# Performance work log

Measured on AMD Instinct MI355X. Metric: run time of the kernel, lower is better.

The kernel has to match this reference:

```python
import jax, jax.numpy as jnp
import numpy as np

LN_EPS = 1e-5


def setup_inputs() -> dict:
    key = jax.random.key(0)
    ks = jax.random.split(key, 4)
    B, S, H, R = 8, 4096, 1024, 64
    hidden_states = jax.random.normal(ks[0], (B, S, H), dtype=jnp.float32)
    w_down = jax.random.normal(ks[1], (H, R), dtype=jnp.float32) * (1.0 / np.sqrt(H))
    b_down = jnp.zeros((R,), dtype=jnp.float32)
    w_up = jax.random.normal(ks[2], (R, H), dtype=jnp.float32) * (1.0 / np.sqrt(R))
    b_up = jnp.zeros((H,), dtype=jnp.float32)
    ln_gamma = jnp.ones((H,), dtype=jnp.float32)
    ln_beta = jnp.zeros((H,), dtype=jnp.float32)
    return {
        "hidden_states": hidden_states,
        "ln_gamma": ln_gamma,
        "ln_beta": ln_beta,
        "w_down": w_down,
        "b_down": b_down,
        "w_up": w_up,
        "b_up": b_up,
    }


def _layernorm(x, gamma, beta):
    mu = jnp.mean(x, axis=-1, keepdims=True)
    var = jnp.mean(jnp.square(x - mu), axis=-1, keepdims=True)
    return (x - mu) * jax.lax.rsqrt(var + LN_EPS) * gamma + beta


def reference(hidden_states, ln_gamma, ln_beta, w_down, b_down, w_up, b_up):
    # pre-norm adapter: LN -> down-proj -> gelu -> up-proj -> +residual
    res = hidden_states
    h = _layernorm(hidden_states, ln_gamma, ln_beta)
    h = jnp.einsum("bsh,hr->bsr", h, w_down) + b_down
    h = jax.nn.gelu(h, approximate=False)  # torch GELU (exact erf form)
    h = jnp.einsum("bsr,rh->bsh", h, w_up) + b_up
    return h + res
```

## Files before the change

kernel.cpp:

```cpp
#include <hip/hip_runtime.h>
#include <hip/hip_bf16.h>
#include <math.h>

#define H 1024
#define R 64
#define BM 16
#define NTHREADS 256
#define TSTRIDE 72

typedef __attribute__((ext_vector_type(8))) short short8;
typedef __attribute__((ext_vector_type(4))) float floatx4;

__device__ __forceinline__ unsigned short f2bf(float f) {
    unsigned int u = __builtin_bit_cast(unsigned int, f);
    u += 0x7fffu + ((u >> 16) & 1u);
    return (unsigned short)(u >> 16);
}

__global__ void prep_weights(const float* __restrict__ w_down,
                             const float* __restrict__ w_up,
                             unsigned short* __restrict__ wsd,
                             unsigned short* __restrict__ wsu) {
    int tid = blockIdx.x * blockDim.x + threadIdx.x;
    int j    = tid & 7;
    int lane = (tid >> 3) & 63;
    int f    = tid >> 9;
    int b = lane >> 4, p = lane & 15;
    {
        int kk = f >> 2, n = f & 3;
        int row = kk * 32 + b * 8 + j;
        int col = n * 16 + p;
        wsd[tid] = f2bf(w_down[row * R + col]);
    }
    {
        int ks = f >> 6, n = f & 63;
        int row = ks * 32 + b * 8 + j;
        int col = n * 16 + p;
        wsu[tid] = f2bf(w_up[row * H + col]);
    }
}

__global__ __launch_bounds__(NTHREADS, 4)
void adapter_kernel(const float* __restrict__ x,
                    const float* __restrict__ gamma,
                    const float* __restrict__ beta,
                    const float* __restrict__ b_down,
                    const float* __restrict__ b_up,
                    const unsigned short* __restrict__ wsd,
                    const unsigned short* __restrict__ wsu,
                    float* __restrict__ out) {
    __shared__ __align__(16) unsigned short y_lds[BM * H];
    __shared__ __align__(16) unsigned short t_lds[BM * TSTRIDE];

    const int tid  = threadIdx.x;
    const int lane = tid & 63;
    const int wave = tid >> 6;
    const long rowbase = (long)blockIdx.x * BM;

    float gg[16], bb[16];
    {
        const floatx4* g4 = (const floatx4*)(gamma + lane * 16);
        const floatx4* b4 = (const floatx4*)(beta  + lane * 16);
        #pragma unroll
        for (int q = 0; q < 4; ++q) {
            floatx4 gv = g4[q], bv = b4[q];
            #pragma unroll
            for (int e = 0; e < 4; ++e) { gg[q*4+e] = gv[e]; bb[q*4+e] = bv[e]; }
        }
    }
    #pragma unroll 2
    for (int i = 0; i < 4; ++i) {
        int r = wave * 4 + i;
        const floatx4* xr = (const floatx4*)(x + (rowbase + r) * H + lane * 16);
        float v[16];
        #pragma unroll
        for (int q = 0; q < 4; ++q) {
            floatx4 xv = xr[q];
            #pragma unroll
            for (int e = 0; e < 4; ++e) v[q*4+e] = xv[e];
        }
        float s1 = 0.f, s2 = 0.f;
        #pragma unroll
        for (int q = 0; q < 16; ++q) { s1 += v[q]; s2 += v[q] * v[q]; }
        #pragma unroll
        for (int off = 32; off >= 1; off >>= 1) {
            s1 += __shfl_xor(s1, off);
            s2 += __shfl_xor(s2, off);
        }
        float mu  = s1 * (1.0f / (float)H);
        float var = s2 * (1.0f / (float)H) - mu * mu;
        float rs  = rsqrtf(var + 1e-5f);
        int c = r & 7;
        short8 lo, hi;
        #pragma unroll
        for (int q = 0; q < 8; ++q) lo[q] = (short)f2bf((v[q]     - mu) * rs * gg[q]     + bb[q]);
        #pragma unroll
        for (int q = 0; q < 8; ++q) hi[q] = (short)f2bf((v[q + 8] - mu) * rs * gg[q + 8] + bb[q + 8]);
        int s0  = (2 * lane)     ^ c;
        int s1g = (2 * lane + 1) ^ c;
        *(short8*)&y_lds[r * H + s0  * 8] = lo;
        *(short8*)&y_lds[r * H + s1g * 8] = hi;
    }
    __syncthreads();

    const int p = lane & 15;
    const int b = lane >> 4;

    floatx4 acc = {0.f, 0.f, 0.f, 0.f};
    const int asw = p & 7;
    const short8* wsd8 = (const short8*)wsd;
    #pragma unroll 4
    for (int kk = 0; kk < 32; ++kk) {
        int gidx = 4 * kk + b;
        short8 a  = *(const short8*)&y_lds[p * H + ((gidx ^ asw) * 8)];
        short8 b0 = wsd8[(kk * 4 + wave) * 64 + lane];
        acc = __builtin_amdgcn_mfma_f32_16x16x32_bf16(a, b0, acc, 0, 0, 0);
    }
    {
        float bd = b_down[16 * wave + p];
        #pragma unroll
        for (int reg = 0; reg < 4; ++reg) {
            int trow = b * 4 + reg;
            float u = acc[reg] + bd;
            u = 0.5f * u * (1.0f + erff(u * 0.70710678f));
            t_lds[trow * TSTRIDE + 16 * wave + p] = f2bf(u);
        }
    }
    __syncthreads();

    short8 a0 = *(const short8*)&t_lds[p * TSTRIDE + b * 8];
    short8 a1 = *(const short8*)&t_lds[p * TSTRIDE + 32 + b * 8];
    const short8* wsu8 = (const short8*)wsu;

    #pragma unroll 2
    for (int nn = 0; nn < 16; ++nn) {
        int n = 16 * wave + nn;
        short8 bu0 = wsu8[(n)      * 64 + lane];
        short8 bu1 = wsu8[(64 + n) * 64 + lane];
        floatx4 av = {0.f, 0.f, 0.f, 0.f};
        av = __builtin_amdgcn_mfma_f32_16x16x32_bf16(a0, bu0, av, 0, 0, 0);
        av = __builtin_amdgcn_mfma_f32_16x16x32_bf16(a1, bu1, av, 0, 0, 0);
        int col = n * 16 + p;
        float bup = b_up[col];
        #pragma unroll
        for (int reg = 0; reg < 4; ++reg) {
            long rr = rowbase + b * 4 + reg;
            out[rr * H + col] = av[reg] + bup + x[rr * H + col];
        }
    }
}

extern "C" void kernel_launch(void* const* d_in, const int* in_sizes, int n_in,
                              void* d_out, int out_size, void* d_ws, size_t ws_size,
                              hipStream_t stream) {
    const float* x      = (const float*)d_in[0];
    const float* gamma  = (const float*)d_in[1];
    const float* beta   = (const float*)d_in[2];
    const float* w_down = (const float*)d_in[3];
    const float* b_down = (const float*)d_in[4];
    const float* w_up   = (const float*)d_in[5];
    const float* b_up   = (const float*)d_in[6];
    float* out = (float*)d_out;

    unsigned short* wsd = (unsigned short*)d_ws;
    unsigned short* wsu = wsd + 65536;

    int M = in_sizes[0] / H;
    prep_weights<<<256, 256, 0, stream>>>(w_down, w_up, wsd, wsu);
    adapter_kernel<<<M / BM, NTHREADS, 0, stream>>>(x, gamma, beta, b_down, b_up,
                                                    wsd, wsu, out);
}
```

Measured before the change: 268.7 us.

## Fold LayerNorm into down-projection weights and split K across waves

Rewrites the down-projection so the raw input x (in bf16) multiplies gamma-scaled weights directly, and applies LayerNorm algebraically afterward as rs*(acc - mu*sum(gamma*w)) + (beta*w + b_down). The normalized row no longer has to be written to and read back from LDS. Each wave now handles a quarter of the hidden dimension for all 64 rows, with partial sums reduced through LDS. The block tile grows from 16 to 64 rows and occupancy drops to 2 blocks per SM. Rounding raw x to bf16 before subtracting the mean, together with the single-pass variance, may cost accuracy when inputs have a large mean.

After: 279.4 us. 1.04x slower.

```diff
diff --git a/kernel.cpp b/kernel.cpp
--- a/kernel.cpp
+++ b/kernel.cpp
@@ -4,9 +4,10 @@
 
 #define H 1024
 #define R 64
-#define BM 16
+#define BM 64
 #define NTHREADS 256
 #define TSTRIDE 72
+#define PSTRIDE 20
 
 typedef __attribute__((ext_vector_type(8))) short short8;
 typedef __attribute__((ext_vector_type(4))) float floatx4;
@@ -19,6 +20,7 @@
 
 __global__ void prep_weights(const float* __restrict__ w_down,
                              const float* __restrict__ w_up,
+                             const float* __restrict__ gamma,
                              unsigned short* __restrict__ wsd,
                              unsigned short* __restrict__ wsu) {
     int tid = blockIdx.x * blockDim.x + threadIdx.x;
@@ -30,7 +32,7 @@
         int kk = f >> 2, n = f & 3;
         int row = kk * 32 + b * 8 + j;
         int col = n * 16 + p;
-        wsd[tid] = f2bf(w_down[row * R + col]);
+        wsd[tid] = f2bf(gamma[row] * w_down[row * R + col]);
     }
     {
         int ks = f >> 6, n = f & 63;
@@ -40,112 +42,176 @@
     }
 }
 
-__global__ __launch_bounds__(NTHREADS, 4)
+__global__ void prep_vec(const float* __restrict__ w_down,
+                         const float* __restrict__ gamma,
+                         const float* __restrict__ beta,
+                         const float* __restrict__ b_down,
+                         float* __restrict__ w1, float* __restrict__ c0) {
+    int r = blockIdx.x;
+    int t = threadIdx.x;
+    float a = 0.f, c = 0.f;
+    for (int h = t; h < H; h += NTHREADS) {
+        float wd = w_down[h * R + r];
+        a += gamma[h] * wd;
+        c += beta[h] * wd;
+    }
+    #pragma unroll
+    for (int off = 32; off >= 1; off >>= 1) {
+        a += __shfl_xor(a, off);
+        c += __shfl_xor(c, off);
+    }
+    __shared__ float red[8];
+    int wv = t >> 6;
+    if ((t & 63) == 0) { red[wv] = a; red[4 + wv] = c; }
+    __syncthreads();
+    if (t == 0) {
+        w1[r] = red[0] + red[1] + red[2] + red[3];
+        c0[r] = red[4] + red[5] + red[6] + red[7] + b_down[r];
+    }
+}
+
+__global__ __launch_bounds__(NTHREADS, 2)
 void adapter_kernel(const float* __restrict__ x,
-                    const float* __restrict__ gamma,
-                    const float* __restrict__ beta,
-                    const float* __restrict__ b_down,
                     const float* __restrict__ b_up,
                     const unsigned short* __restrict__ wsd,
                     const unsigned short* __restrict__ wsu,
+                    const float* __restrict__ w1v,
+                    const float* __restrict__ c0v,
                     float* __restrict__ out) {
-    __shared__ __align__(16) unsigned short y_lds[BM * H];
+    __shared__ __align__(16) float part[12 * 64 * PSTRIDE];
     __shared__ __align__(16) unsigned short t_lds[BM * TSTRIDE];
+    __shared__ float s1w[4][BM], s2w[4][BM];
 
     const int tid  = threadIdx.x;
     const int lane = tid & 63;
-    const int wave = tid >> 6;
+    const int w    = tid >> 6;
+    const int p    = lane & 15;
+    const int b    = lane >> 4;
     const long rowbase = (long)blockIdx.x * BM;
-
-    float gg[16], bb[16];
-    {
-        const floatx4* g4 = (const floatx4*)(gamma + lane * 16);
-        const floatx4* b4 = (const floatx4*)(beta  + lane * 16);
-        #pragma unroll
-        for (int q = 0; q < 4; ++q) {
-            floatx4 gv = g4[q], bv = b4[q];
-            #pragma unroll
-            for (int e = 0; e < 4; ++e) { gg[q*4+e] = gv[e]; bb[q*4+e] = bv[e]; }
-        }
-    }
-    #pragma unroll 2
-    for (int i = 0; i < 4; ++i) {
-        int r = wave * 4 + i;
-        const floatx4* xr = (const floatx4*)(x + (rowbase + r) * H + lane * 16);
-        float v[16];
-        #pragma unroll
-        for (int q = 0; q < 4; ++q) {
-            floatx4 xv = xr[q];
-            #pragma unroll
-            for (int e = 0; e < 4; ++e) v[q*4+e] = xv[e];
-        }
-        float s1 = 0.f, s2 = 0.f;
-        #pragma unroll
-        for (int q = 0; q < 16; ++q) { s1 += v[q]; s2 += v[q] * v[q]; }
-        #pragma unroll
-        for (int off = 32; off >= 1; off >>= 1) {
-            s1 += __shfl_xor(s1, off);
-            s2 += __shfl_xor(s2, off);
-        }
-        float mu  = s1 * (1.0f / (float)H);
-        float var = s2 * (1.0f / (float)H) - mu * mu;
-        float rs  = rsqrtf(var + 1e-5f);
-        int c = r & 7;
-        short8 lo, hi;
-        #pragma unroll
-        for (int q = 0; q < 8; ++q) lo[q] = (short)f2bf((v[q]     - mu) * rs * gg[q]     + bb[q]);
-        #pragma unroll
-        for (int q = 0; q < 8; ++q) hi[q] = (short)f2bf((v[q + 8] - mu) * rs * gg[q + 8] + bb[q + 8]);
-        int s0  = (2 * lane)     ^ c;
-        int s1g = (2 * lane + 1) ^ c;
-        *(short8*)&y_lds[r * H + s0  * 8] = lo;
-        *(short8*)&y_lds[r * H + s1g * 8] = hi;
+    const int kbase = w * 256;
+
+    float s1[4] = {0.f,0.f,0.f,0.f}, s2[4] = {0.f,0.f,0.f,0.f};
+    floatx4 acc[4][4];
+    #pragma unroll
+    for (int mt = 0; mt < 4; ++mt)
+        #pragma unroll
+        for (int nt = 0; nt < 4; ++nt)
+            acc[mt][nt] = floatx4{0.f,0.f,0.f,0.f};
+
+    const short8* wsd8 = (const short8*)wsd;
+    #pragma unroll
+    for (int kt = 0; kt < 8; ++kt) {
+        short8 af[4];
+        #pragma unroll
+        for (int mt = 0; mt < 4; ++mt) {
+            const float* px = x + (rowbase + mt * 16 + p) * H + kbase + kt * 32 + b * 8;
+            floatx4 v0 = *(const floatx4*)px;
+            floatx4 v1 = *(const floatx4*)(px + 4);
+            short8 a;
+            #pragma unroll
+            for (int e = 0; e < 4; ++e) {
+                s1[mt] += v0[e] + v1[e];
+                s2[mt] += v0[e] * v0[e] + v1[e] * v1[e];
+                a[e]     = (short)f2bf(v0[e]);
+                a[4 + e] = (short)f2bf(v1[e]);
+            }
+            af[mt] = a;
+        }
+        #pragma unroll
+        for (int nt = 0; nt < 4; ++nt) {
+            short8 bfrag = wsd8[(size_t)((w * 8 + kt) * 4 + nt) * 64 + lane];
+            #pragma unroll
+            for (int mt = 0; mt < 4; ++mt)
+                acc[mt][nt] = __builtin_amdgcn_mfma_f32_16x16x32_bf16(af[mt], bfrag, acc[mt][nt], 0, 0, 0);
+        }
+    }
+
+    #pragma unroll
+    for (int mt = 0; mt < 4; ++mt) {
+        s1[mt] += __shfl_xor(s1[mt], 16); s1[mt] += __shfl_xor(s1[mt], 32);
+        s2[mt] += __shfl_xor(s2[mt], 16); s2[mt] += __shfl_xor(s2[mt], 32);
+    }
+    if (b == 0) {
+        #pragma unroll
+        for (int mt = 0; mt < 4; ++mt) {
+            s1w[w][mt * 16 + p] = s1[mt];
+            s2w[w][mt * 16 + p] = s2[mt];
+        }
+    }
+
+    floatx4 own[4];
+    #pragma unroll
+    for (int mt = 0; mt < 4; ++mt) {
+        if (mt != w) {
+            int idx = w * 3 + (mt < w ? mt : mt - 1);
+            float* dst = &part[idx * 64 * PSTRIDE];
+            #pragma unroll
+            for (int nt = 0; nt < 4; ++nt)
+                *(floatx4*)&dst[(nt * 16 + p) * PSTRIDE + b * 4] = acc[mt][nt];
+        } else {
+            #pragma unroll
+            for (int nt = 0; nt < 4; ++nt) own[nt] = acc[mt][nt];
+        }
     }
     __syncthreads();
 
-    const int p = lane & 15;
-    const int b = lane >> 4;
-
-    floatx4 acc = {0.f, 0.f, 0.f, 0.f};
-    const int asw = p & 7;
-    const short8* wsd8 = (const short8*)wsd;
-    #pragma unroll 4
-    for (int kk = 0; kk < 32; ++kk) {
-        int gidx = 4 * kk + b;
-        short8 a  = *(const short8*)&y_lds[p * H + ((gidx ^ asw) * 8)];
-        short8 b0 = wsd8[(kk * 4 + wave) * 64 + lane];
-        acc = __builtin_amdgcn_mfma_f32_16x16x32_bf16(a, b0, acc, 0, 0, 0);
-    }
-    {
-        float bd = b_down[16 * wave + p];
+    #pragma unroll
+    for (int src = 0; src < 3; ++src) {
+        int ow  = (src < w) ? src : src + 1;
+        int idx = ow * 3 + (w < ow ? w : w - 1);
+        const float* sp = &part[idx * 64 * PSTRIDE];
+        #pragma unroll
+        for (int nt = 0; nt < 4; ++nt)
+            own[nt] += *(const floatx4*)&sp[(nt * 16 + p) * PSTRIDE + b * 4];
+    }
+    float mu[4], rs[4];
+    #pragma unroll
+    for (int reg = 0; reg < 4; ++reg) {
+        int row = w * 16 + b * 4 + reg;
+        float a = s1w[0][row] + s1w[1][row] + s1w[2][row] + s1w[3][row];
+        float q = s2w[0][row] + s2w[1][row] + s2w[2][row] + s2w[3][row];
+        float m = a * (1.0f / (float)H);
+        float var = q * (1.0f / (float)H) - m * m;
+        mu[reg] = m;
+        rs[reg] = rsqrtf(var + 1e-5f);
+    }
+    #pragma unroll
+    for (int nt = 0; nt < 4; ++nt) {
+        float wv1 = w1v[nt * 16 + p];
+        float cv0 = c0v[nt * 16 + p];
         #pragma unroll
         for (int reg = 0; reg < 4; ++reg) {
-            int trow = b * 4 + reg;
-            float u = acc[reg] + bd;
+            float u = rs[reg] * (own[nt][reg] - mu[reg] * wv1) + cv0;
             u = 0.5f * u * (1.0f + erff(u * 0.70710678f));
-            t_lds[trow * TSTRIDE + 16 * wave + p] = f2bf(u);
+            t_lds[(w * 16 + b * 4 + reg) * TSTRIDE + nt * 16 + p] = f2bf(u);
         }
     }
     __syncthreads();
 
-    short8 a0 = *(const short8*)&t_lds[p * TSTRIDE + b * 8];
-    short8 a1 = *(const short8*)&t_lds[p * TSTRIDE + 32 + b * 8];
+    short8 a0[4], a1[4];
+    #pragma unroll
+    for (int mt = 0; mt < 4; ++mt) {
+        a0[mt] = *(const short8*)&t_lds[(mt * 16 + p) * TSTRIDE + b * 8];
+        a1[mt] = *(const short8*)&t_lds[(mt * 16 + p) * TSTRIDE + 32 + b * 8];
+    }
     const short8* wsu8 = (const short8*)wsu;
-
     #pragma unroll 2
     for (int nn = 0; nn < 16; ++nn) {
-        int n = 16 * wave + nn;
-        short8 bu0 = wsu8[(n)      * 64 + lane];
-        short8 bu1 = wsu8[(64 + n) * 64 + lane];
-        floatx4 av = {0.f, 0.f, 0.f, 0.f};
-        av = __builtin_amdgcn_mfma_f32_16x16x32_bf16(a0, bu0, av, 0, 0, 0);
-        av = __builtin_amdgcn_mfma_f32_16x16x32_bf16(a1, bu1, av, 0, 0, 0);
+        int n = w * 16 + nn;
+        short8 bu0 = wsu8[(size_t)n * 64 + lane];
+        short8 bu1 = wsu8[(size_t)(64 + n) * 64 + lane];
         int col = n * 16 + p;
         float bup = b_up[col];
         #pragma unroll
-        for (int reg = 0; reg < 4; ++reg) {
-            long rr = rowbase + b * 4 + reg;
-            out[rr * H + col] = av[reg] + bup + x[rr * H + col];
+        for (int mt = 0; mt < 4; ++mt) {
+            floatx4 av = {0.f, 0.f, 0.f, 0.f};
+            av = __builtin_amdgcn_mfma_f32_16x16x32_bf16(a0[mt], bu0, av, 0, 0, 0);
+            av = __builtin_amdgcn_mfma_f32_16x16x32_bf16(a1[mt], bu1, av, 0, 0, 0);
+            #pragma unroll
+            for (int reg = 0; reg < 4; ++reg) {
+                long rr = rowbase + mt * 16 + b * 4 + reg;
+                out[rr * H + col] = av[reg] + bup + x[rr * H + col];
+            }
         }
     }
 }
@@ -164,9 +230,11 @@
 
     unsigned short* wsd = (unsigned short*)d_ws;
     unsigned short* wsu = wsd + 65536;
+    float* w1 = (float*)(wsu + 65536);
+    float* c0 = w1 + 64;
 
     int M = in_sizes[0] / H;
-    prep_weights<<<256, 256, 0, stream>>>(w_down, w_up, wsd, wsu);
-    adapter_kernel<<<M / BM, NTHREADS, 0, stream>>>(x, gamma, beta, b_down, b_up,
-                                                    wsd, wsu, out);
-}
+    prep_weights<<<256, 256, 0, stream>>>(w_down, w_up, gamma, wsd, wsu);
+    prep_vec<<<64, 256, 0, stream>>>(w_down, gamma, beta, b_down, w1, c0);
+    adapter_kernel<<<M / BM, NTHREADS, 0, stream>>>(x, b_up, wsd, wsu, w1, c0, out);
+}
```

## Fold LayerNorm into down-projection weights and compute GEMM directly from raw input

Applied to the files above, without the earlier changes.

LayerNorm's gamma is folded into the down-projection weights, and beta with the bias into a per-column constant. The down GEMM now runs on raw bf16-converted x, and mean/rstd are applied afterwards as a rank-1 correction (rs*(acc - mu*w1) + c0). This removes the normalized-activation LDS staging buffer and a block barrier. Each wave now owns 16 rows with 64 rows per block, and a new small prep kernel computes the folded vectors. The risk is extra precision loss, because raw x goes to bf16 before the mean is subtracted, so the subtraction happens after the bf16 GEMM.

Result: slower. 289.2 us (+7.6%).

```diff
diff --git a/kernel.cpp b/kernel.cpp
--- a/kernel.cpp
+++ b/kernel.cpp
@@ -4,8 +4,9 @@
 
 #define H 1024
 #define R 64
-#define BM 16
 #define NTHREADS 256
+#define ROWS_PER_WAVE 16
+#define ROWS_PER_BLOCK 64
 #define TSTRIDE 72
 
 typedef __attribute__((ext_vector_type(8))) short short8;
@@ -19,6 +20,7 @@
 
 __global__ void prep_weights(const float* __restrict__ w_down,
                              const float* __restrict__ w_up,
+                             const float* __restrict__ gamma,
                              unsigned short* __restrict__ wsd,
                              unsigned short* __restrict__ wsu) {
     int tid = blockIdx.x * blockDim.x + threadIdx.x;
@@ -30,7 +32,7 @@
         int kk = f >> 2, n = f & 3;
         int row = kk * 32 + b * 8 + j;
         int col = n * 16 + p;
-        wsd[tid] = f2bf(w_down[row * R + col]);
+        wsd[tid] = f2bf(gamma[row] * w_down[row * R + col]);
     }
     {
         int ks = f >> 6, n = f & 63;
@@ -40,103 +42,104 @@
     }
 }
 
+__global__ void prep_vec(const float* __restrict__ w_down,
+                         const float* __restrict__ gamma,
+                         const float* __restrict__ beta,
+                         const float* __restrict__ b_down,
+                         float* __restrict__ w1, float* __restrict__ c0) {
+    int r = blockIdx.x;
+    int t = threadIdx.x;
+    float a = 0.f, c = 0.f;
+    for (int h = t; h < H; h += NTHREADS) {
+        float wd = w_down[h * R + r];
+        a += gamma[h] * wd;
+        c += beta[h] * wd;
+    }
+    #pragma unroll
+    for (int off = 32; off >= 1; off >>= 1) {
+        a += __shfl_xor(a, off);
+        c += __shfl_xor(c, off);
+    }
+    __shared__ float red[8];
+    int wv = t >> 6;
+    if ((t & 63) == 0) { red[wv] = a; red[4 + wv] = c; }
+    __syncthreads();
+    if (t == 0) {
+        w1[r] = red[0] + red[1] + red[2] + red[3];
+        c0[r] = red[4] + red[5] + red[6] + red[7] + b_down[r];
+    }
+}
+
 __global__ __launch_bounds__(NTHREADS, 4)
 void adapter_kernel(const float* __restrict__ x,
-                    const float* __restrict__ gamma,
-                    const float* __restrict__ beta,
-                    const float* __restrict__ b_down,
                     const float* __restrict__ b_up,
                     const unsigned short* __restrict__ wsd,
                     const unsigned short* __restrict__ wsu,
+                    const float* __restrict__ w1v,
+                    const float* __restrict__ c0v,
                     float* __restrict__ out) {
-    __shared__ __align__(16) unsigned short y_lds[BM * H];
-    __shared__ __align__(16) unsigned short t_lds[BM * TSTRIDE];
+    __shared__ __align__(16) unsigned short t_lds[4][ROWS_PER_WAVE * TSTRIDE];
 
     const int tid  = threadIdx.x;
     const int lane = tid & 63;
-    const int wave = tid >> 6;
-    const long rowbase = (long)blockIdx.x * BM;
+    const int w    = tid >> 6;
+    const int p    = lane & 15;
+    const int b    = lane >> 4;
+    const long row0 = (long)blockIdx.x * ROWS_PER_BLOCK + w * ROWS_PER_WAVE;
 
-    float gg[16], bb[16];
-    {
-        const floatx4* g4 = (const floatx4*)(gamma + lane * 16);
-        const floatx4* b4 = (const floatx4*)(beta  + lane * 16);
+    float s1 = 0.f, s2 = 0.f;
+    floatx4 acc[4];
+    #pragma unroll
+    for (int nt = 0; nt < 4; ++nt) acc[nt] = floatx4{0.f, 0.f, 0.f, 0.f};
+
+    const short8* wsd8 = (const short8*)wsd;
+    const float* xw = x + (row0 + p) * H + b * 8;
+    #pragma unroll 4
+    for (int kt = 0; kt < 32; ++kt) {
+        floatx4 v0 = *(const floatx4*)(xw + kt * 32);
+        floatx4 v1 = *(const floatx4*)(xw + kt * 32 + 4);
+        short8 a;
         #pragma unroll
-        for (int q = 0; q < 4; ++q) {
-            floatx4 gv = g4[q], bv = b4[q];
-            #pragma unroll
-            for (int e = 0; e < 4; ++e) { gg[q*4+e] = gv[e]; bb[q*4+e] = bv[e]; }
+        for (int e = 0; e < 4; ++e) {
+            s1 += v0[e] + v1[e];
+            s2 += v0[e] * v0[e] + v1[e] * v1[e];
+            a[e]     = (short)f2bf(v0[e]);
+            a[4 + e] = (short)f2bf(v1[e]);
         }
+        #pragma unroll
+        for (int nt = 0; nt < 4; ++nt)
+            acc[nt] = __builtin_amdgcn_mfma_f32_16x16x32_bf16(a, wsd8[(size_t)(kt * 4 + nt) * 64 + lane], acc[nt], 0, 0, 0);
     }
-    #pragma unroll 2
-    for (int i = 0; i < 4; ++i) {
-        int r = wave * 4 + i;
-        const floatx4* xr = (const floatx4*)(x + (rowbase + r) * H + lane * 16);
-        float v[16];
+
+    s1 += __shfl_xor(s1, 16); s1 += __shfl_xor(s1, 32);
+    s2 += __shfl_xor(s2, 16); s2 += __shfl_xor(s2, 32);
+    float mu = s1 * (1.0f / (float)H);
+    float var = s2 * (1.0f / (float)H) - mu * mu;
+    float rs = rsqrtf(var + 1e-5f);
+
+    #pragma unroll
+    for (int reg = 0; reg < 4; ++reg) {
+        float mur = __shfl(mu, b * 4 + reg);
+        float rsr = __shfl(rs, b * 4 + reg);
         #pragma unroll
-        for (int q = 0; q < 4; ++q) {
-            floatx4 xv = xr[q];
-            #pragma unroll
-            for (int e = 0; e < 4; ++e) v[q*4+e] = xv[e];
-        }
-        float s1 = 0.f, s2 = 0.f;
-        #pragma unroll
-        for (int q = 0; q < 16; ++q) { s1 += v[q]; s2 += v[q] * v[q]; }
-        #pragma unroll
-        for (int off = 32; off >= 1; off >>= 1) {
-            s1 += __shfl_xor(s1, off);
-            s2 += __shfl_xor(s2, off);
-        }
-        float mu  = s1 * (1.0f / (float)H);
-        float var = s2 * (1.0f / (float)H) - mu * mu;
-        float rs  = rsqrtf(var + 1e-5f);
-        int c = r & 7;
-        short8 lo, hi;
-        #pragma unroll
-        for (int q = 0; q < 8; ++q) lo[q] = (short)f2bf((v[q]     - mu) * rs * gg[q]     + bb[q]);
-        #pragma unroll
-        for (int q = 0; q < 8; ++q) hi[q] = (short)f2bf((v[q + 8] - mu) * rs * gg[q + 8] + bb[q + 8]);
-        int s0  = (2 * lane)     ^ c;
-        int s1g = (2 * lane + 1) ^ c;
-        *(short8*)&y_lds[r * H + s0  * 8] = lo;
-        *(short8*)&y_lds[r * H + s1g * 8] = hi;
-    }
-    __syncthreads();
-
-    const int p = lane & 15;
-    const int b = lane >> 4;
-
-    floatx4 acc = {0.f, 0.f, 0.f, 0.f};
-    const int asw = p & 7;
-    const short8* wsd8 = (const short8*)wsd;
-    #pragma unroll 4
-    for (int kk = 0; kk < 32; ++kk) {
-        int gidx = 4 * kk + b;
-        short8 a  = *(const short8*)&y_lds[p * H + ((gidx ^ asw) * 8)];
-        short8 b0 = wsd8[(kk * 4 + wave) * 64 + lane];
-        acc = __builtin_amdgcn_mfma_f32_16x16x32_bf16(a, b0, acc, 0, 0, 0);
-    }
-    {
-        float bd = b_down[16 * wave + p];
-        #pragma unroll
-        for (int reg = 0; reg < 4; ++reg) {
-            int trow = b * 4 + reg;
-            float u = acc[reg] + bd;
+        for (int nt = 0; nt < 4; ++nt) {
+            int col = nt * 16 + p;
+            float u = rsr * (acc[nt][reg] - mur * w1v[col]) + c0v[col];
             u = 0.5f * u * (1.0f + erff(u * 0.70710678f));
-            t_lds[trow * TSTRIDE + 16 * wave + p] = f2bf(u);
+            t_lds[w][(b * 4 + reg) * TSTRIDE + col] = f2bf(u);
         }
     }
     __syncthreads();
 
-    short8 a0 = *(const short8*)&t_lds[p * TSTRIDE + b * 8];
-    short8 a1 = *(const short8*)&t_lds[p * TSTRIDE + 32 + b * 8];
+    short8 a0 = *(const short8*)&t_lds[w][p * TSTRIDE + b * 8];
+    short8 a1 = *(const short8*)&t_lds[w][p * TSTRIDE + 32 + b * 8];
     const short8* wsu8 = (const short8*)wsu;
+    const long rbase = row0 + b * 4;
 
-    #pragma unroll 2
-    for (int nn = 0; nn < 16; ++nn) {
-        int n = 16 * wave + nn;
-        short8 bu0 = wsu8[(n)      * 64 + lane];
-        short8 bu1 = wsu8[(64 + n) * 64 + lane];
+    #pragma unroll 4
+    for (int n = 0; n < 64; ++n) {
+        short8 bu0 = wsu8[(size_t)n * 64 + lane];
+        short8 bu1 = wsu8[(size_t)(64 + n) * 64 + lane];
         floatx4 av = {0.f, 0.f, 0.f, 0.f};
         av = __builtin_amdgcn_mfma_f32_16x16x32_bf16(a0, bu0, av, 0, 0, 0);
         av = __builtin_amdgcn_mfma_f32_16x16x32_bf16(a1, bu1, av, 0, 0, 0);
@@ -144,7 +147,7 @@
         float bup = b_up[col];
         #pragma unroll
         for (int reg = 0; reg < 4; ++reg) {
-            long rr = rowbase + b * 4 + reg;
+            long rr = rbase + reg;
             out[rr * H + col] = av[reg] + bup + x[rr * H + col];
         }
     }
@@ -164,9 +167,11 @@
 
     unsigned short* wsd = (unsigned short*)d_ws;
     unsigned short* wsu = wsd + 65536;
+    float* w1 = (float*)(wsu + 65536);
+    float* c0 = w1 + 64;
 
     int M = in_sizes[0] / H;
-    prep_weights<<<256, 256, 0, stream>>>(w_down, w_up, wsd, wsu);
-    adapter_kernel<<<M / BM, NTHREADS, 0, stream>>>(x, gamma, beta, b_down, b_up,
-                                                    wsd, wsu, out);
+    prep_weights<<<256, 256, 0, stream>>>(w_down, w_up, gamma, wsd, wsu);
+    prep_vec<<<64, 256, 0, stream>>>(w_down, gamma, beta, b_down, w1, c0);
+    adapter_kernel<<<M / ROWS_PER_BLOCK, NTHREADS, 0, stream>>>(x, b_up, wsd, wsu, w1, c0, out);
 }
```
